# Kernel tuning notes

Measured on AMD Instinct MI355X. Metric: run time of the kernel, lower is better.

## Reference

```python
import jax, jax.numpy as jnp
import numpy as np

DIM = 128
L = 4
EPS = 1e-5


def setup_inputs() -> dict:
    key = jax.random.key(0)
    ks = jax.random.split(key, 16)
    g, n_per = 4096, 32
    n = g * n_per
    e = 4 * n
    s = 0.05
    inp = {
        "x_atoms": jax.random.randint(ks[0], (n, 2), 0, 3),
        "edge_index": jax.random.randint(ks[1], (2, e), 0, n),
        "edge_attr": jax.random.randint(ks[2], (e, 2), 0, 3),
        "batch": jnp.repeat(jnp.arange(g), n_per),
        "num_graphs": g,
        "max_nodes": n_per,
        "task_embs": jax.random.normal(ks[3], (g, DIM), jnp.float32),
        "teb": jax.random.normal(ks[4], (g, DIM), jnp.float32),
        "emb1": jax.random.normal(ks[5], (120, DIM), jnp.float32) * s,
        "emb2": jax.random.normal(ks[6], (3, DIM), jnp.float32) * s,
        "edge_e1": jax.random.normal(ks[7], (L, 6, DIM), jnp.float32) * s,
        "edge_e2": jax.random.normal(ks[8], (L, 3, DIM), jnp.float32) * s,
        "W1": jax.random.normal(ks[9], (L, DIM, 2 * DIM), jnp.float32) * s,
        "b1": jnp.zeros((L, 2 * DIM), jnp.float32),
        "W2": jax.random.normal(ks[10], (L, 2 * DIM, DIM), jnp.float32) * s,
        "b2": jnp.zeros((L, DIM), jnp.float32),
        "bn_w": jnp.ones((L, DIM), jnp.float32),
        "bn_b": jnp.zeros((L, DIM), jnp.float32),
        "film_Wg": jax.random.normal(ks[11], (2, DIM, DIM), jnp.float32) * s,
        "film_bg": jnp.zeros((2, DIM), jnp.float32),
        "film_Wb": jax.random.normal(ks[12], (2, DIM, DIM), jnp.float32) * s,
        "film_bb": jnp.zeros((2, DIM), jnp.float32),
    }
    return inp


def _gin_layer(x, src, dst, eattr, e1, e2, W1, b1, W2, b2):
    # GINConv (pretrain-gnns): scatter-add of (x_j + edge_emb) + self-loop (attr [4,0]), then 2-layer MLP.
    n = x.shape[0]
    emb = e1[eattr[:, 0]] + e2[eattr[:, 1]]                       # [E, D]
    agg = jax.ops.segment_sum(x[src] + emb, dst, num_segments=n)  # [N, D]
    agg = agg + x + (e1[4] + e2[0])                               # self loops
    h = jax.nn.relu(agg @ W1 + b1)
    return h @ W2 + b2


def _batchnorm(x, w, b):
    mu = jnp.mean(x, axis=0)
    var = jnp.var(x, axis=0)
    return (x - mu) * jax.lax.rsqrt(var + EPS) * w + b


def reference(x_atoms, edge_index, edge_attr, batch, num_graphs, max_nodes,
              task_embs, teb, emb1, emb2, edge_e1, edge_e2,
              W1, b1, W2, b2, bn_w, bn_b,
              film_Wg, film_bg, film_Wb, film_bb):
    g = int(num_graphs)
    n = x_atoms.shape[0]
    x = emb1[x_atoms[:, 0]] + emb2[x_atoms[:, 1]]                 # [N, D]
    # --- add virtual nodes (one per graph) and bidirectional virtual edges ---
    x = jnp.concatenate([x, teb], axis=0)                         # [N+g, D]
    dst0 = jnp.arange(n)
    vsrc = n + batch                                              # virtual node index per real node
    src_all = jnp.concatenate([edge_index[0], vsrc, dst0])
    dst_all = jnp.concatenate([edge_index[1], dst0, vsrc])
    v_attr = jnp.tile(jnp.array([[5, 0]], dtype=edge_attr.dtype), (2 * n, 1))
    eattr = jnp.concatenate([edge_attr, v_attr], axis=0)
    # --- positions within graph for to_dense_batch (batch is sorted) ---
    counts = jnp.bincount(batch, length=g)
    offsets = jnp.cumsum(counts) - counts
    pos = dst0 - offsets[batch]
    for layer in range(L):
        x = _gin_layer(x, src_all, dst_all, eattr,
                       edge_e1[layer], edge_e2[layer],
                       W1[layer], b1[layer], W2[layer], b2[layer])
        if layer in (1, 3):
            xv = x[n:]
            dense = jnp.zeros((g, int(max_nodes), DIM), x.dtype).at[batch, pos].set(x[:n])
            fl = layer // 3
            gamma = task_embs @ film_Wg[fl] + film_bg[fl]          # [g, D]
            beta = task_embs @ film_Wb[fl] + film_bb[fl]
            dense = gamma[:, None, :] * dense + beta[:, None, :]
            x = jnp.concatenate([dense[batch, pos], xv], axis=0)   # masked_select inverse
        x = _batchnorm(x, bn_w[layer], bn_b[layer])
        if layer != L - 1:
            x = jax.nn.relu(x)
        # dropout is identity in eval mode
    return x[:n]
```

## Files before the change

kernel.cpp:

```cpp
#include <hip/hip_runtime.h>
#include <hip/hip_bf16.h>

typedef __bf16 bf16_t;
typedef bf16_t bf16x8 __attribute__((ext_vector_type(8)));
typedef float f32x4 __attribute__((ext_vector_type(4)));

#define EPSV 1e-5f

__global__ void k_zerof(float* p, int cnt) {
  int i = blockIdx.x * 256 + threadIdx.x;
  if (i < cnt) p[i] = 0.f;
}
__global__ void k_zeroi(int* p, int cnt) {
  int i = blockIdx.x * 256 + threadIdx.x;
  if (i < cnt) p[i] = 0;
}

__global__ void k_prep_weights(const float* __restrict__ W1, const float* __restrict__ W2,
                               bf16_t* __restrict__ W1T, bf16_t* __restrict__ W2T, int total) {
  int idx = blockIdx.x * 256 + threadIdx.x;
  if (idx >= total) return;
  int l = idx >> 15, r = idx & 32767;
  int k = r >> 8, c = r & 255;
  W1T[(l << 15) + c * 128 + k] = (bf16_t)W1[idx];
  int k2 = r >> 7, c2 = r & 127;
  W2T[(l << 15) + c2 * 256 + k2] = (bf16_t)W2[idx];
}

__global__ void k_prep_film(const float* __restrict__ Wg, const float* __restrict__ Wb,
                            bf16_t* __restrict__ fWT) {
  int idx = blockIdx.x * 256 + threadIdx.x;
  if (idx >= 4 * 16384) return;
  int m = idx >> 14, r = idx & 16383;
  int c = r >> 7, k = r & 127;
  const float* W = ((m & 1) ? Wb : Wg) + (m >> 1) * 16384;
  fWT[idx] = (bf16_t)W[k * 128 + c];
}

__global__ void k_prep_te(const float* __restrict__ te, bf16_t* __restrict__ teb_out, int total) {
  int idx = blockIdx.x * 256 + threadIdx.x;
  if (idx < total) teb_out[idx] = (bf16_t)te[idx];
}

__global__ void k_ecomb(const float* __restrict__ e1, const float* __restrict__ e2,
                        float* __restrict__ ec, int total) {
  int idx = blockIdx.x * 256 + threadIdx.x;
  if (idx >= total) return;
  int ch = idx & 127;
  int t = idx >> 7;
  int comb = t % 18, l = t / 18;
  int i = comb / 3, j = comb % 3;
  ec[idx] = e1[(l * 6 + i) * 128 + ch] + e2[(l * 3 + j) * 128 + ch];
}

__launch_bounds__(256, 2)
__global__ void k_film(const bf16_t* __restrict__ teb, const bf16_t* __restrict__ fWT,
                       const float* __restrict__ bg, const float* __restrict__ bb,
                       float* __restrict__ gbuf, int g) {
  const int mat = blockIdx.x & 3;
  const int r0 = (blockIdx.x >> 2) * 64;
  const int tid = threadIdx.x;
  const int wave = tid >> 6, lane = tid & 63;
  const int lr = lane & 15, lk = lane >> 4;
  const int w32 = wave * 32;
  const bf16_t* W = fWT + mat * 16384;
  const float* B = ((mat & 1) ? bb : bg) + (mat >> 1) * 128;

  bf16x8 bbf[2][4];
  #pragma unroll
  for (int cf = 0; cf < 2; ++cf)
    #pragma unroll
    for (int kk = 0; kk < 4; ++kk)
      bbf[cf][kk] = *(const bf16x8*)(W + ((w32 + cf * 16 + lr) << 7) + kk * 32 + (lk << 3));

  f32x4 acc[4][2];
  f32x4 zero4 = {0.f, 0.f, 0.f, 0.f};
  #pragma unroll
  for (int rf = 0; rf < 4; ++rf)
    #pragma unroll
    for (int cf = 0; cf < 2; ++cf) acc[rf][cf] = zero4;

  #pragma unroll
  for (int kk = 0; kk < 4; ++kk) {
    bf16x8 a[4];
    #pragma unroll
    for (int rf = 0; rf < 4; ++rf)
      a[rf] = *(const bf16x8*)(teb + ((size_t)(r0 + rf * 16 + lr) << 7) + kk * 32 + (lk << 3));
    #pragma unroll
    for (int rf = 0; rf < 4; ++rf)
      #pragma unroll
      for (int cf = 0; cf < 2; ++cf)
        acc[rf][cf] = __builtin_amdgcn_mfma_f32_16x16x32_bf16(a[rf], bbf[cf][kk], acc[rf][cf], 0, 0, 0);
  }

  float* out = gbuf + (size_t)mat * g * 128;
  #pragma unroll
  for (int cf = 0; cf < 2; ++cf) {
    int col = w32 + cf * 16 + lr;
    float bias = B[col];
    #pragma unroll
    for (int rf = 0; rf < 4; ++rf)
      #pragma unroll
      for (int j = 0; j < 4; ++j) {
        int row = r0 + rf * 16 + lk * 4 + j;
        out[(size_t)row * 128 + col] = acc[rf][cf][j] + bias;
      }
  }
}

__global__ void k_init_x(const int* __restrict__ xa, const float* __restrict__ teb,
                         const float* __restrict__ emb1, const float* __restrict__ emb2,
                         bf16_t* __restrict__ x, int n, int N) {
  int idx = blockIdx.x * 256 + threadIdx.x;
  if (idx >= N * 128) return;
  int row = idx >> 7, ch = idx & 127;
  float v;
  if (row < n) v = emb1[xa[row * 2] * 128 + ch] + emb2[xa[row * 2 + 1] * 128 + ch];
  else v = teb[(size_t)(row - n) * 128 + ch];
  x[idx] = (bf16_t)v;
}

__global__ void k_hist(const int* __restrict__ eidx, int* __restrict__ cnt, int E) {
  int i = blockIdx.x * 256 + threadIdx.x;
  if (i < E) atomicAdd(&cnt[eidx[E + i]], 1);
}

__global__ void k_scan1(const int* __restrict__ cnt, int* __restrict__ part,
                        int* __restrict__ bsum, int n) {
  __shared__ int s[256];
  int i = blockIdx.x * 256 + threadIdx.x;
  int v = (i < n) ? cnt[i] : 0;
  s[threadIdx.x] = v;
  for (int off = 1; off < 256; off <<= 1) {
    __syncthreads();
    int t = (threadIdx.x >= off) ? s[threadIdx.x - off] : 0;
    __syncthreads();
    s[threadIdx.x] += t;
  }
  __syncthreads();
  if (i < n) part[i] = s[threadIdx.x] - v;
  if (threadIdx.x == 255) bsum[blockIdx.x] = s[255];
}

__global__ void k_scan2(int* bsum, int nb) {
  __shared__ int s[512];
  int v = ((int)threadIdx.x < nb) ? bsum[threadIdx.x] : 0;
  s[threadIdx.x] = v;
  for (int off = 1; off < 512; off <<= 1) {
    __syncthreads();
    int t = ((int)threadIdx.x >= off) ? s[threadIdx.x - off] : 0;
    __syncthreads();
    s[threadIdx.x] += t;
  }
  __syncthreads();
  if ((int)threadIdx.x < nb) bsum[threadIdx.x] = s[threadIdx.x] - v;
}

__global__ void k_scan3(int* __restrict__ rp, const int* __restrict__ bsum,
                        int* __restrict__ fill, int n, int E) {
  int i = blockIdx.x * 256 + threadIdx.x;
  if (i < n) {
    int v = rp[i] + bsum[i >> 8];
    rp[i] = v;
    fill[i] = v;
  }
  if (i == 0) rp[n] = E;
}

__global__ void k_scatter(const int* __restrict__ eidx, const int* __restrict__ eattr,
                          int* __restrict__ fill, int* __restrict__ pack, int E) {
  int i = blockIdx.x * 256 + threadIdx.x;
  if (i >= E) return;
  int s = eidx[i];
  int d = eidx[E + i];
  int comb = eattr[2 * i] * 3 + eattr[2 * i + 1];
  int p = atomicAdd(&fill[d], 1);
  pack[p] = s | (comb << 20);
}

__global__ void k_normx(const bf16_t* __restrict__ y, const float* __restrict__ scsh,
                        bf16_t* __restrict__ xn, int total8) {
  int i = blockIdx.x * 256 + threadIdx.x;
  if (i >= total8) return;
  int ch8 = i & 15;
  bf16x8 v = ((const bf16x8*)y)[i];
  float4 sc0 = ((const float4*)scsh)[ch8 * 2];
  float4 sc1 = ((const float4*)scsh)[ch8 * 2 + 1];
  float4 sh0 = ((const float4*)(scsh + 128))[ch8 * 2];
  float4 sh1 = ((const float4*)(scsh + 128))[ch8 * 2 + 1];
  float sc[8] = {sc0.x, sc0.y, sc0.z, sc0.w, sc1.x, sc1.y, sc1.z, sc1.w};
  float sh[8] = {sh0.x, sh0.y, sh0.z, sh0.w, sh1.x, sh1.y, sh1.z, sh1.w};
  bf16x8 o;
  #pragma unroll
  for (int j = 0; j < 8; ++j)
    o[j] = (bf16_t)fmaxf(fmaf((float)v[j], sc[j], sh[j]), 0.f);
  ((bf16x8*)xn)[i] = o;
}

__global__ void k_agg(const bf16_t* __restrict__ xn, const int* __restrict__ batch,
                      const int* __restrict__ rp, const int* __restrict__ pack,
                      const float* __restrict__ ec,
                      bf16_t* __restrict__ agg, int n, int N, int npg) {
  int node = blockIdx.x * 16 + (threadIdx.x >> 4);
  if (node >= N) return;
  const int lane = threadIdx.x & 63;
  const int li = lane & 15;
  const int grpl = lane & 48;
  const int ch0 = li * 8;

  float4 s0 = *(const float4*)(ec + 12 * 128 + ch0);
  float4 s1 = *(const float4*)(ec + 12 * 128 + ch0 + 4);
  float4 v0 = *(const float4*)(ec + 15 * 128 + ch0);
  float4 v1 = *(const float4*)(ec + 15 * 128 + ch0 + 4);
  bf16x8 hs = *(const bf16x8*)(xn + ((size_t)node << 7) + ch0);
  float acc[8];

  if (node < n) {
    int b = batch[node];
    bf16x8 hv = *(const bf16x8*)(xn + ((size_t)(n + b) << 7) + ch0);
    acc[0] = (float)hs[0] + (float)hv[0] + s0.x + v0.x;
    acc[1] = (float)hs[1] + (float)hv[1] + s0.y + v0.y;
    acc[2] = (float)hs[2] + (float)hv[2] + s0.z + v0.z;
    acc[3] = (float)hs[3] + (float)hv[3] + s0.w + v0.w;
    acc[4] = (float)hs[4] + (float)hv[4] + s1.x + v1.x;
    acc[5] = (float)hs[5] + (float)hv[5] + s1.y + v1.y;
    acc[6] = (float)hs[6] + (float)hv[6] + s1.z + v1.z;
    acc[7] = (float)hs[7] + (float)hv[7] + s1.w + v1.w;
    int beg = rp[node], end = rp[node + 1];
    for (int base = beg; base < end; base += 16) {
      int cnt = end - base; if (cnt > 16) cnt = 16;
      int pl = pack[base + (li < cnt ? li : cnt - 1)];
      for (int j0 = 0; j0 < cnt; j0 += 4) {
        bf16x8 hx[4]; float4 e0[4], e1[4]; float m[4];
        #pragma unroll
        for (int u = 0; u < 4; ++u) {
          int j = j0 + u;
          int jj = j < cnt ? j : cnt - 1;
          m[u] = (j < cnt) ? 1.f : 0.f;
          int p = __shfl(pl, grpl | jj, 64);
          hx[u] = *(const bf16x8*)(xn + ((size_t)(p & 0xFFFFF) << 7) + ch0);
          const float* er = ec + ((p >> 20) & 31) * 128 + ch0;
          e0[u] = *(const float4*)er;
          e1[u] = *(const float4*)(er + 4);
        }
        #pragma unroll
        for (int u = 0; u < 4; ++u) {
          acc[0] = fmaf(m[u], (float)hx[u][0] + e0[u].x, acc[0]);
          acc[1] = fmaf(m[u], (float)hx[u][1] + e0[u].y, acc[1]);
          acc[2] = fmaf(m[u], (float)hx[u][2] + e0[u].z, acc[2]);
          acc[3] = fmaf(m[u], (float)hx[u][3] + e0[u].w, acc[3]);
          acc[4] = fmaf(m[u], (float)hx[u][4] + e1[u].x, acc[4]);
          acc[5] = fmaf(m[u], (float)hx[u][5] + e1[u].y, acc[5]);
          acc[6] = fmaf(m[u], (float)hx[u][6] + e1[u].z, acc[6]);
          acc[7] = fmaf(m[u], (float)hx[u][7] + e1[u].w, acc[7]);
        }
      }
    }
  } else {
    float fn = (float)npg;
    acc[0] = (float)hs[0] + s0.x + fn * v0.x;
    acc[1] = (float)hs[1] + s0.y + fn * v0.y;
    acc[2] = (float)hs[2] + s0.z + fn * v0.z;
    acc[3] = (float)hs[3] + s0.w + fn * v0.w;
    acc[4] = (float)hs[4] + s1.x + fn * v1.x;
    acc[5] = (float)hs[5] + s1.y + fn * v1.y;
    acc[6] = (float)hs[6] + s1.z + fn * v1.z;
    acc[7] = (float)hs[7] + s1.w + fn * v1.w;
    int base = (node - n) * npg;
    for (int k = 0; k < npg; k += 4) {
      bf16x8 hx[4];
      #pragma unroll
      for (int u = 0; u < 4; ++u)
        hx[u] = *(const bf16x8*)(xn + ((size_t)(base + k + u) << 7) + ch0);
      #pragma unroll
      for (int u = 0; u < 4; ++u)
        #pragma unroll
        for (int j = 0; j < 8; ++j) acc[j] += (float)hx[u][j];
    }
  }

  bf16x8 o;
  #pragma unroll
  for (int j = 0; j < 8; ++j) o[j] = (bf16_t)acc[j];
  *(bf16x8*)(agg + ((size_t)node << 7) + ch0) = o;
}

__launch_bounds__(512, 4)
__global__ void k_mlp(const bf16_t* __restrict__ agg, const bf16_t* __restrict__ W1T,
                      const bf16_t* __restrict__ W2T, const float* __restrict__ b1,
                      const float* __restrict__ b2, const float* __restrict__ gamma,
                      const float* __restrict__ beta, const int* __restrict__ batch,
                      bf16_t* __restrict__ y, float* __restrict__ gstats, int n, int N) {
  __shared__ __align__(16) char As[16384];
  __shared__ __align__(16) char Hs[32768];
  __shared__ float sred[256];
  const int tid = threadIdx.x;
  const int m0 = blockIdx.x * 64;
  const int wave = tid >> 6, lane = tid & 63;
  const int lr = lane & 15, lk = lane >> 4;
  if (tid < 256) sred[tid] = 0.f;

  #pragma unroll
  for (int it = 0; it < 2; ++it) {
    int e = it * 512 + tid;
    int row = e >> 4, c16 = e & 15;
    bf16x8 v = *(const bf16x8*)(agg + ((size_t)(m0 + row) << 7) + c16 * 8);
    int byte = (row << 8) + (c16 << 4);
    byte ^= (row & 7) << 4;
    *(bf16x8*)(As + byte) = v;
  }

  const int c1base = wave * 32;
  bf16x8 bb1[2][4];
  #pragma unroll
  for (int cf = 0; cf < 2; ++cf)
    #pragma unroll
    for (int kk = 0; kk < 4; ++kk)
      bb1[cf][kk] = *(const bf16x8*)(W1T + ((c1base + cf * 16 + lr) << 7) + kk * 32 + (lk << 3));

  __syncthreads();

  f32x4 zero4 = {0.f, 0.f, 0.f, 0.f};
  f32x4 acc1[4][2];
  #pragma unroll
  for (int rf = 0; rf < 4; ++rf)
    #pragma unroll
    for (int cf = 0; cf < 2; ++cf) acc1[rf][cf] = zero4;

  #pragma unroll
  for (int kk = 0; kk < 4; ++kk) {
    bf16x8 a[4];
    #pragma unroll
    for (int rf = 0; rf < 4; ++rf) {
      int arow = rf * 16 + lr;
      int abyte = (arow << 8) + kk * 64 + (lk << 4);
      abyte ^= (arow & 7) << 4;
      a[rf] = *(const bf16x8*)(As + abyte);
    }
    #pragma unroll
    for (int rf = 0; rf < 4; ++rf)
      #pragma unroll
      for (int cf = 0; cf < 2; ++cf)
        acc1[rf][cf] = __builtin_amdgcn_mfma_f32_16x16x32_bf16(a[rf], bb1[cf][kk], acc1[rf][cf], 0, 0, 0);
  }

  #pragma unroll
  for (int cf = 0; cf < 2; ++cf) {
    int col = c1base + cf * 16 + lr;
    float bias = b1[col];
    #pragma unroll
    for (int rf = 0; rf < 4; ++rf)
      #pragma unroll
      for (int j = 0; j < 4; ++j) {
        int r = rf * 16 + lk * 4 + j;
        float h = acc1[rf][cf][j] + bias;
        h = h > 0.f ? h : 0.f;
        int byte = (r << 9) + col * 2;
        byte ^= (r & 15) << 4;
        *(bf16_t*)(Hs + byte) = (bf16_t)h;
      }
  }

  const int c2base = wave * 16;
  bf16x8 bb2[8];
  #pragma unroll
  for (int kk = 0; kk < 8; ++kk)
    bb2[kk] = *(const bf16x8*)(W2T + ((c2base + lr) << 8) + kk * 32 + (lk << 3));

  __syncthreads();

  f32x4 acc2[4];
  #pragma unroll
  for (int rf = 0; rf < 4; ++rf) acc2[rf] = zero4;

  #pragma unroll
  for (int kk = 0; kk < 8; ++kk) {
    bf16x8 a2[4];
    #pragma unroll
    for (int rf = 0; rf < 4; ++rf) {
      int row = rf * 16 + lr;
      int byte = (row << 9) + kk * 64 + (lk << 4);
      byte ^= (row & 15) << 4;
      a2[rf] = *(const bf16x8*)(Hs + byte);
    }
    #pragma unroll
    for (int rf = 0; rf < 4; ++rf)
      acc2[rf] = __builtin_amdgcn_mfma_f32_16x16x32_bf16(a2[rf], bb2[kk], acc2[rf], 0, 0, 0);
  }

  int gb[4][4];
  #pragma unroll
  for (int rf = 0; rf < 4; ++rf)
    #pragma unroll
    for (int j = 0; j < 4; ++j) {
      int row = m0 + rf * 16 + lk * 4 + j;
      gb[rf][j] = (gamma != nullptr && row < n) ? batch[row] : -1;
    }

  {
    int col = c2base + lr;
    float bias = b2[col];
    float s = 0.f, q = 0.f;
    #pragma unroll
    for (int rf = 0; rf < 4; ++rf)
      #pragma unroll
      for (int j = 0; j < 4; ++j) {
        int row = m0 + rf * 16 + lk * 4 + j;
        float v = acc2[rf][j] + bias;
        if (gb[rf][j] >= 0)
          v = gamma[(size_t)gb[rf][j] * 128 + col] * v + beta[(size_t)gb[rf][j] * 128 + col];
        y[(size_t)row * 128 + col] = (bf16_t)v;
        s += v; q += v * v;
      }
    s += __shfl_xor(s, 16, 64); s += __shfl_xor(s, 32, 64);
    q += __shfl_xor(q, 16, 64); q += __shfl_xor(q, 32, 64);
    if (lane < 16) { sred[col] = s; sred[128 + col] = q; }
  }
  __syncthreads();
  if (tid < 256) atomicAdd(&gstats[((blockIdx.x & 15) << 8) + tid], sred[tid]);
}

__global__ void k_finalize(float* st, const float* __restrict__ bnw,
                           const float* __restrict__ bnb, float invN) {
  int ch = threadIdx.x;
  float s = 0.f, q = 0.f;
  #pragma unroll
  for (int c = 0; c < 16; ++c) { s += st[c * 256 + ch]; q += st[c * 256 + 128 + ch]; }
  __syncthreads();
  #pragma unroll
  for (int z = 0; z < 32; ++z) st[ch * 32 + z] = 0.f;
  float mean = s * invN;
  float var = fmaxf(q * invN - mean * mean, 0.f);
  float inv = rsqrtf(var + EPSV);
  float sc = inv * bnw[ch];
  st[4096 + ch] = sc;
  st[4224 + ch] = bnb[ch] - mean * sc;
}

__global__ void k_norm(const bf16_t* __restrict__ yin, const float* __restrict__ scsh,
                       float* __restrict__ out, int total8) {
  int i = blockIdx.x * 256 + threadIdx.x;
  if (i >= total8) return;
  int ch8 = i & 15;
  bf16x8 v = ((const bf16x8*)yin)[i];
  float4 sc0 = ((const float4*)scsh)[ch8 * 2];
  float4 sc1 = ((const float4*)scsh)[ch8 * 2 + 1];
  float4 sh0 = ((const float4*)(scsh + 128))[ch8 * 2];
  float4 sh1 = ((const float4*)(scsh + 128))[ch8 * 2 + 1];
  float4 r0, r1;
  r0.x = (float)v[0] * sc0.x + sh0.x;
  r0.y = (float)v[1] * sc0.y + sh0.y;
  r0.z = (float)v[2] * sc0.z + sh0.z;
  r0.w = (float)v[3] * sc0.w + sh0.w;
  r1.x = (float)v[4] * sc1.x + sh1.x;
  r1.y = (float)v[5] * sc1.y + sh1.y;
  r1.z = (float)v[6] * sc1.z + sh1.z;
  r1.w = (float)v[7] * sc1.w + sh1.w;
  ((float4*)out)[i * 2] = r0;
  ((float4*)out)[i * 2 + 1] = r1;
}

extern "C" void kernel_launch(void* const* d_in, const int* in_sizes, int n_in,
                              void* d_out, int out_size, void* d_ws, size_t ws_size,
                              hipStream_t stream) {
  const int*   x_atoms    = (const int*)d_in[0];
  const int*   edge_index = (const int*)d_in[1];
  const int*   edge_attr  = (const int*)d_in[2];
  const int*   batch      = (const int*)d_in[3];
  const float* task_embs  = (const float*)d_in[6];
  const float* teb        = (const float*)d_in[7];
  const float* emb1       = (const float*)d_in[8];
  const float* emb2       = (const float*)d_in[9];
  const float* edge_e1    = (const float*)d_in[10];
  const float* edge_e2    = (const float*)d_in[11];
  const float* W1         = (const float*)d_in[12];
  const float* b1         = (const float*)d_in[13];
  const float* W2         = (const float*)d_in[14];
  const float* b2         = (const float*)d_in[15];
  const float* bnw        = (const float*)d_in[16];
  const float* bnb        = (const float*)d_in[17];
  const float* fWg        = (const float*)d_in[18];
  const float* fbg        = (const float*)d_in[19];
  const float* fWb        = (const float*)d_in[20];
  const float* fbb        = (const float*)d_in[21];

  const int n   = in_sizes[0] / 2;
  const int E   = in_sizes[1] / 2;
  const int g   = in_sizes[6] / 128;
  const int N   = n + g;
  const int npg = n / g;
  const int L   = in_sizes[12] / 32768;

  char* ws = (char*)d_ws;
  size_t off = 0;
  auto alloc = [&](size_t bytes) { size_t o = off; off += (bytes + 255) & ~(size_t)255; return o; };
  bf16_t* xbuf   = (bf16_t*)(ws + alloc((size_t)N * 128 * 2));
  bf16_t* xn     = (bf16_t*)(ws + alloc((size_t)N * 128 * 2));
  bf16_t* aggb   = (bf16_t*)(ws + alloc((size_t)N * 128 * 2));
  float*  gbuf   = (float*)(ws + alloc((size_t)4 * g * 128 * 4));
  bf16_t* W1Tb   = (bf16_t*)(ws + alloc((size_t)L * 32768 * 2));
  bf16_t* W2Tb   = (bf16_t*)(ws + alloc((size_t)L * 32768 * 2));
  bf16_t* fWTb   = (bf16_t*)(ws + alloc((size_t)4 * 16384 * 2));
  bf16_t* tebuf  = (bf16_t*)(ws + alloc((size_t)g * 128 * 2));
  float*  ecomb  = (float*)(ws + alloc((size_t)L * 18 * 128 * 4));
  float*  gstats = (float*)(ws + alloc((size_t)(4096 + 256) * 4));
  int*    row_ptr= (int*)(ws + alloc((size_t)(n + 1) * 4));
  int*    fill   = (int*)(ws + alloc((size_t)n * 4));
  int*    epack  = (int*)(ws + alloc((size_t)E * 4));
  int*    bsum   = (int*)(ws + alloc(512 * 4));
  (void)ws_size; (void)n_in; (void)out_size;

  k_prep_weights<<<(L * 32768 + 255) / 256, 256, 0, stream>>>(W1, W2, W1Tb, W2Tb, L * 32768);
  k_prep_film<<<(4 * 16384 + 255) / 256, 256, 0, stream>>>(fWg, fWb, fWTb);
  k_prep_te<<<(g * 128 + 255) / 256, 256, 0, stream>>>(task_embs, tebuf, g * 128);
  k_init_x<<<(N * 128 + 255) / 256, 256, 0, stream>>>(x_atoms, teb, emb1, emb2, xn, n, N);
  k_ecomb<<<(L * 18 * 128 + 255) / 256, 256, 0, stream>>>(edge_e1, edge_e2, ecomb, L * 18 * 128);
  k_film<<<(g / 64) * 4, 256, 0, stream>>>(tebuf, fWTb, fbg, fbb, gbuf, g);

  const int nb = (n + 255) / 256;
  k_zeroi<<<nb, 256, 0, stream>>>(fill, n);
  k_hist<<<(E + 255) / 256, 256, 0, stream>>>(edge_index, fill, E);
  k_scan1<<<nb, 256, 0, stream>>>(fill, row_ptr, bsum, n);
  k_scan2<<<1, 512, 0, stream>>>(bsum, nb);
  k_scan3<<<nb, 256, 0, stream>>>(row_ptr, bsum, fill, n, E);
  k_scatter<<<(E + 255) / 256, 256, 0, stream>>>(edge_index, edge_attr, fill, epack, E);

  k_zerof<<<16, 256, 0, stream>>>(gstats, 4096);
  for (int l = 0; l < 4; ++l) {
    if (l > 0)
      k_normx<<<(N * 16 + 255) / 256, 256, 0, stream>>>(xbuf, gstats + 4096, xn, N * 16);
    k_agg<<<(N + 15) / 16, 256, 0, stream>>>(xn, batch, row_ptr, epack,
        ecomb + (size_t)l * 18 * 128, aggb, n, N, npg);
    const float* gm = nullptr; const float* bt = nullptr;
    if (l == 1) { gm = gbuf;                       bt = gbuf + (size_t)g * 128; }
    if (l == 3) { gm = gbuf + (size_t)2 * g * 128; bt = gbuf + (size_t)3 * g * 128; }
    k_mlp<<<(N + 63) / 64, 512, 0, stream>>>(aggb, W1Tb + (size_t)l * 32768,
        W2Tb + (size_t)l * 32768, b1 + l * 256, b2 + l * 128, gm, bt, batch,
        xbuf, gstats, n, N);
    k_finalize<<<1, 128, 0, stream>>>(gstats, bnw + l * 128, bnb + l * 128, 1.0f / (float)N);
  }
  k_norm<<<(n * 16 + 255) / 256, 256, 0, stream>>>(xbuf, gstats + 4096, (float*)d_out, n * 16);
}
```

Before: 531.8 us.

## Make MLP kernel persistent with double-buffered prefetch of next input tile

Turns the fused two-layer MLP kernel into a grid-stride persistent kernel capped at 512 blocks. W1 fragments are loaded once per block, and the next 64-row tile of aggregated features is prefetched into registers and written to a second shared-memory buffer while the current tile's epilogue runs. The aim is to amortise weight loads and hide global-load latency behind MFMA work. In exchange it doubles the input-tile shared memory, which may reduce occupancy, and adds row bounds checks.

```diff
diff --git a/kernel.cpp b/kernel.cpp
--- a/kernel.cpp
+++ b/kernel.cpp
@@ -290,25 +290,16 @@
                       const bf16_t* __restrict__ W2T, const float* __restrict__ b1,
                       const float* __restrict__ b2, const float* __restrict__ gamma,
                       const float* __restrict__ beta, const int* __restrict__ batch,
-                      bf16_t* __restrict__ y, float* __restrict__ gstats, int n, int N) {
-  __shared__ __align__(16) char As[16384];
+                      bf16_t* __restrict__ y, float* __restrict__ gstats,
+                      int n, int N, int ntiles) {
+  __shared__ __align__(16) char As[2][16384];
   __shared__ __align__(16) char Hs[32768];
   __shared__ float sred[256];
   const int tid = threadIdx.x;
-  const int m0 = blockIdx.x * 64;
   const int wave = tid >> 6, lane = tid & 63;
   const int lr = lane & 15, lk = lane >> 4;
-  if (tid < 256) sred[tid] = 0.f;
-
-  #pragma unroll
-  for (int it = 0; it < 2; ++it) {
-    int e = it * 512 + tid;
-    int row = e >> 4, c16 = e & 15;
-    bf16x8 v = *(const bf16x8*)(agg + ((size_t)(m0 + row) << 7) + c16 * 8);
-    int byte = (row << 8) + (c16 << 4);
-    byte ^= (row & 7) << 4;
-    *(bf16x8*)(As + byte) = v;
-  }
+  const int srow = tid >> 4;
+  const int sc16 = tid & 15;
 
   const int c1base = wave * 32;
   bf16x8 bb1[2][4];
@@ -317,107 +308,148 @@
     #pragma unroll
     for (int kk = 0; kk < 4; ++kk)
       bb1[cf][kk] = *(const bf16x8*)(W1T + ((c1base + cf * 16 + lr) << 7) + kk * 32 + (lk << 3));
-
+  const int c2base = wave * 16;
+
+  int t = blockIdx.x;
+  {
+    int m0 = t * 64;
+    #pragma unroll
+    for (int it = 0; it < 2; ++it) {
+      int row = it * 32 + srow;
+      int r = m0 + row; r = r < N ? r : N - 1;
+      bf16x8 v = *(const bf16x8*)(agg + ((size_t)r << 7) + sc16 * 8);
+      int byte = (row << 8) + (sc16 << 4);
+      byte ^= (row & 7) << 4;
+      *(bf16x8*)(As[0] + byte) = v;
+    }
+  }
   __syncthreads();
 
   f32x4 zero4 = {0.f, 0.f, 0.f, 0.f};
-  f32x4 acc1[4][2];
-  #pragma unroll
-  for (int rf = 0; rf < 4; ++rf)
-    #pragma unroll
-    for (int cf = 0; cf < 2; ++cf) acc1[rf][cf] = zero4;
-
-  #pragma unroll
-  for (int kk = 0; kk < 4; ++kk) {
-    bf16x8 a[4];
-    #pragma unroll
-    for (int rf = 0; rf < 4; ++rf) {
-      int arow = rf * 16 + lr;
-      int abyte = (arow << 8) + kk * 64 + (lk << 4);
-      abyte ^= (arow & 7) << 4;
-      a[rf] = *(const bf16x8*)(As + abyte);
-    }
+  int cur = 0;
+  for (; t < ntiles; t += gridDim.x) {
+    const int m0 = t * 64;
+
+    f32x4 acc1[4][2];
     #pragma unroll
     for (int rf = 0; rf < 4; ++rf)
       #pragma unroll
-      for (int cf = 0; cf < 2; ++cf)
-        acc1[rf][cf] = __builtin_amdgcn_mfma_f32_16x16x32_bf16(a[rf], bb1[cf][kk], acc1[rf][cf], 0, 0, 0);
-  }
-
-  #pragma unroll
-  for (int cf = 0; cf < 2; ++cf) {
-    int col = c1base + cf * 16 + lr;
-    float bias = b1[col];
-    #pragma unroll
-    for (int rf = 0; rf < 4; ++rf)
-      #pragma unroll
-      for (int j = 0; j < 4; ++j) {
-        int r = rf * 16 + lk * 4 + j;
-        float h = acc1[rf][cf][j] + bias;
-        h = h > 0.f ? h : 0.f;
-        int byte = (r << 9) + col * 2;
-        byte ^= (r & 15) << 4;
-        *(bf16_t*)(Hs + byte) = (bf16_t)h;
-      }
-  }
-
-  const int c2base = wave * 16;
-  bf16x8 bb2[8];
-  #pragma unroll
-  for (int kk = 0; kk < 8; ++kk)
-    bb2[kk] = *(const bf16x8*)(W2T + ((c2base + lr) << 8) + kk * 32 + (lk << 3));
-
-  __syncthreads();
-
-  f32x4 acc2[4];
-  #pragma unroll
-  for (int rf = 0; rf < 4; ++rf) acc2[rf] = zero4;
-
-  #pragma unroll
-  for (int kk = 0; kk < 8; ++kk) {
-    bf16x8 a2[4];
-    #pragma unroll
-    for (int rf = 0; rf < 4; ++rf) {
-      int row = rf * 16 + lr;
-      int byte = (row << 9) + kk * 64 + (lk << 4);
-      byte ^= (row & 15) << 4;
-      a2[rf] = *(const bf16x8*)(Hs + byte);
-    }
-    #pragma unroll
-    for (int rf = 0; rf < 4; ++rf)
-      acc2[rf] = __builtin_amdgcn_mfma_f32_16x16x32_bf16(a2[rf], bb2[kk], acc2[rf], 0, 0, 0);
-  }
-
-  int gb[4][4];
-  #pragma unroll
-  for (int rf = 0; rf < 4; ++rf)
-    #pragma unroll
-    for (int j = 0; j < 4; ++j) {
-      int row = m0 + rf * 16 + lk * 4 + j;
-      gb[rf][j] = (gamma != nullptr && row < n) ? batch[row] : -1;
-    }
-
-  {
-    int col = c2base + lr;
-    float bias = b2[col];
-    float s = 0.f, q = 0.f;
+      for (int cf = 0; cf < 2; ++cf) acc1[rf][cf] = zero4;
+    #pragma unroll
+    for (int kk = 0; kk < 4; ++kk) {
+      bf16x8 a[4];
+      #pragma unroll
+      for (int rf = 0; rf < 4; ++rf) {
+        int arow = rf * 16 + lr;
+        int abyte = (arow << 8) + kk * 64 + (lk << 4);
+        abyte ^= (arow & 7) << 4;
+        a[rf] = *(const bf16x8*)(As[cur] + abyte);
+      }
+      #pragma unroll
+      for (int rf = 0; rf < 4; ++rf)
+        #pragma unroll
+        for (int cf = 0; cf < 2; ++cf)
+          acc1[rf][cf] = __builtin_amdgcn_mfma_f32_16x16x32_bf16(a[rf], bb1[cf][kk], acc1[rf][cf], 0, 0, 0);
+    }
+
+    #pragma unroll
+    for (int cf = 0; cf < 2; ++cf) {
+      int col = c1base + cf * 16 + lr;
+      float bias = b1[col];
+      #pragma unroll
+      for (int rf = 0; rf < 4; ++rf)
+        #pragma unroll
+        for (int j = 0; j < 4; ++j) {
+          int r = rf * 16 + lk * 4 + j;
+          float h = acc1[rf][cf][j] + bias;
+          h = h > 0.f ? h : 0.f;
+          int byte = (r << 9) + col * 2;
+          byte ^= (r & 15) << 4;
+          *(bf16_t*)(Hs + byte) = (bf16_t)h;
+        }
+    }
+
+    bf16x8 bb2[8];
+    #pragma unroll
+    for (int kk = 0; kk < 8; ++kk)
+      bb2[kk] = *(const bf16x8*)(W2T + ((c2base + lr) << 8) + kk * 32 + (lk << 3));
+
+    __syncthreads();
+
+    f32x4 acc2[4];
+    #pragma unroll
+    for (int rf = 0; rf < 4; ++rf) acc2[rf] = zero4;
+    #pragma unroll
+    for (int kk = 0; kk < 8; ++kk) {
+      bf16x8 a2[4];
+      #pragma unroll
+      for (int rf = 0; rf < 4; ++rf) {
+        int row = rf * 16 + lr;
+        int byte = (row << 9) + kk * 64 + (lk << 4);
+        byte ^= (row & 15) << 4;
+        a2[rf] = *(const bf16x8*)(Hs + byte);
+      }
+      #pragma unroll
+      for (int rf = 0; rf < 4; ++rf)
+        acc2[rf] = __builtin_amdgcn_mfma_f32_16x16x32_bf16(a2[rf], bb2[kk], acc2[rf], 0, 0, 0);
+    }
+
+    int tn = t + gridDim.x;
+    bf16x8 st[2];
+    if (tn < ntiles) {
+      int m0n = tn * 64;
+      #pragma unroll
+      for (int it = 0; it < 2; ++it) {
+        int row = it * 32 + srow;
+        int r = m0n + row; r = r < N ? r : N - 1;
+        st[it] = *(const bf16x8*)(agg + ((size_t)r << 7) + sc16 * 8);
+      }
+    }
+
+    int gb[4][4];
     #pragma unroll
     for (int rf = 0; rf < 4; ++rf)
       #pragma unroll
       for (int j = 0; j < 4; ++j) {
         int row = m0 + rf * 16 + lk * 4 + j;
-        float v = acc2[rf][j] + bias;
-        if (gb[rf][j] >= 0)
-          v = gamma[(size_t)gb[rf][j] * 128 + col] * v + beta[(size_t)gb[rf][j] * 128 + col];
-        y[(size_t)row * 128 + col] = (bf16_t)v;
-        s += v; q += v * v;
-      }
-    s += __shfl_xor(s, 16, 64); s += __shfl_xor(s, 32, 64);
-    q += __shfl_xor(q, 16, 64); q += __shfl_xor(q, 32, 64);
-    if (lane < 16) { sred[col] = s; sred[128 + col] = q; }
-  }
-  __syncthreads();
-  if (tid < 256) atomicAdd(&gstats[((blockIdx.x & 15) << 8) + tid], sred[tid]);
+        gb[rf][j] = (gamma != nullptr && row < n) ? batch[row] : -1;
+      }
+    {
+      int col = c2base + lr;
+      float bias = b2[col];
+      float s = 0.f, q = 0.f;
+      #pragma unroll
+      for (int rf = 0; rf < 4; ++rf)
+        #pragma unroll
+        for (int j = 0; j < 4; ++j) {
+          int row = m0 + rf * 16 + lk * 4 + j;
+          if (row < N) {
+            float v = acc2[rf][j] + bias;
+            if (gb[rf][j] >= 0)
+              v = gamma[(size_t)gb[rf][j] * 128 + col] * v + beta[(size_t)gb[rf][j] * 128 + col];
+            y[(size_t)row * 128 + col] = (bf16_t)v;
+            s += v; q += v * v;
+          }
+        }
+      s += __shfl_xor(s, 16, 64); s += __shfl_xor(s, 32, 64);
+      q += __shfl_xor(q, 16, 64); q += __shfl_xor(q, 32, 64);
+      if (lane < 16) { sred[col] = s; sred[128 + col] = q; }
+    }
+
+    if (tn < ntiles) {
+      #pragma unroll
+      for (int it = 0; it < 2; ++it) {
+        int row = it * 32 + srow;
+        int byte = (row << 8) + (sc16 << 4);
+        byte ^= (row & 7) << 4;
+        *(bf16x8*)(As[cur ^ 1] + byte) = st[it];
+      }
+    }
+    __syncthreads();
+
+    if (tid < 256) atomicAdd(&gstats[((t & 15) << 8) + tid], sred[tid]);
+    cur ^= 1;
+  }
 }
 
 __global__ void k_finalize(float* st, const float* __restrict__ bnw,
@@ -490,13 +522,14 @@
   const int N   = n + g;
   const int npg = n / g;
   const int L   = in_sizes[12] / 32768;
+  const int ntiles = (N + 63) / 64;
 
   char* ws = (char*)d_ws;
   size_t off = 0;
   auto alloc = [&](size_t bytes) { size_t o = off; off += (bytes + 255) & ~(size_t)255; return o; };
   bf16_t* xbuf   = (bf16_t*)(ws + alloc((size_t)N * 128 * 2));
   bf16_t* xn     = (bf16_t*)(ws + alloc((size_t)N * 128 * 2));
-  bf16_t* aggb   = (bf16_t*)(ws + alloc((size_t)N * 128 * 2));
+  bf16_t* aggb   = (bf16_t*)(ws + alloc((size_t)(ntiles * 64) * 128 * 2));
   float*  gbuf   = (float*)(ws + alloc((size_t)4 * g * 128 * 4));
   bf16_t* W1Tb   = (bf16_t*)(ws + alloc((size_t)L * 32768 * 2));
   bf16_t* W2Tb   = (bf16_t*)(ws + alloc((size_t)L * 32768 * 2));
@@ -526,6 +559,7 @@
   k_scatter<<<(E + 255) / 256, 256, 0, stream>>>(edge_index, edge_attr, fill, epack, E);
 
   k_zerof<<<16, 256, 0, stream>>>(gstats, 4096);
+  const int mlp_grid = (ntiles < 512) ? ntiles : 512;
   for (int l = 0; l < 4; ++l) {
     if (l > 0)
       k_normx<<<(N * 16 + 255) / 256, 256, 0, stream>>>(xbuf, gstats + 4096, xn, N * 16);
@@ -534,9 +568,9 @@
     const float* gm = nullptr; const float* bt = nullptr;
     if (l == 1) { gm = gbuf;                       bt = gbuf + (size_t)g * 128; }
     if (l == 3) { gm = gbuf + (size_t)2 * g * 128; bt = gbuf + (size_t)3 * g * 128; }
-    k_mlp<<<(N + 63) / 64, 512, 0, stream>>>(aggb, W1Tb + (size_t)l * 32768,
+    k_mlp<<<mlp_grid, 512, 0, stream>>>(aggb, W1Tb + (size_t)l * 32768,
         W2Tb + (size_t)l * 32768, b1 + l * 256, b2 + l * 128, gm, bt, batch,
-        xbuf, gstats, n, N);
+        xbuf, gstats, n, N, ntiles);
     k_finalize<<<1, 128, 0, stream>>>(gstats, bnw + l * 128, bnb + l * 128, 1.0f / (float)N);
   }
   k_norm<<<(n * 16 + 255) / 256, 256, 0, stream>>>(xbuf, gstats + 4096, (float*)d_out, n * 16);
```

After: 1.082 ms. +103.4%, slower.

## Fuse batchnorm+ReLU into aggregation gather and merge prep kernels

Applied to the files above, without the earlier changes.

Removes the separate normalize-and-ReLU pass that wrote a normalized copy of x each layer, and instead applies the batchnorm scale/shift and ReLU on the fly inside the aggregation kernel on every gathered neighbor row. This saves one full read and write of the N×128 activation per layer and three kernel launches per forward. The cost is extra FMAs per gathered edge, since each node is normalized about five times instead of once. It also merges the four small weight and embedding prep kernels into a single launch.

```diff
diff --git a/kernel.cpp b/kernel.cpp
--- a/kernel.cpp
+++ b/kernel.cpp
@@ -16,41 +16,41 @@
   if (i < cnt) p[i] = 0;
 }
 
-__global__ void k_prep_weights(const float* __restrict__ W1, const float* __restrict__ W2,
-                               bf16_t* __restrict__ W1T, bf16_t* __restrict__ W2T, int total) {
+__global__ void k_prep_all(const float* __restrict__ W1, const float* __restrict__ W2,
+                           bf16_t* __restrict__ W1T, bf16_t* __restrict__ W2T,
+                           const float* __restrict__ Wg, const float* __restrict__ Wb,
+                           bf16_t* __restrict__ fWT,
+                           const float* __restrict__ te, bf16_t* __restrict__ teb,
+                           const float* __restrict__ e1, const float* __restrict__ e2,
+                           float* __restrict__ ec, int L, int g) {
   int idx = blockIdx.x * 256 + threadIdx.x;
-  if (idx >= total) return;
-  int l = idx >> 15, r = idx & 32767;
-  int k = r >> 8, c = r & 255;
-  W1T[(l << 15) + c * 128 + k] = (bf16_t)W1[idx];
-  int k2 = r >> 7, c2 = r & 127;
-  W2T[(l << 15) + c2 * 256 + k2] = (bf16_t)W2[idx];
-}
-
-__global__ void k_prep_film(const float* __restrict__ Wg, const float* __restrict__ Wb,
-                            bf16_t* __restrict__ fWT) {
-  int idx = blockIdx.x * 256 + threadIdx.x;
-  if (idx >= 4 * 16384) return;
-  int m = idx >> 14, r = idx & 16383;
-  int c = r >> 7, k = r & 127;
-  const float* W = ((m & 1) ? Wb : Wg) + (m >> 1) * 16384;
-  fWT[idx] = (bf16_t)W[k * 128 + c];
-}
-
-__global__ void k_prep_te(const float* __restrict__ te, bf16_t* __restrict__ teb_out, int total) {
-  int idx = blockIdx.x * 256 + threadIdx.x;
-  if (idx < total) teb_out[idx] = (bf16_t)te[idx];
-}
-
-__global__ void k_ecomb(const float* __restrict__ e1, const float* __restrict__ e2,
-                        float* __restrict__ ec, int total) {
-  int idx = blockIdx.x * 256 + threadIdx.x;
-  if (idx >= total) return;
-  int ch = idx & 127;
-  int t = idx >> 7;
-  int comb = t % 18, l = t / 18;
-  int i = comb / 3, j = comb % 3;
-  ec[idx] = e1[(l * 6 + i) * 128 + ch] + e2[(l * 3 + j) * 128 + ch];
+  int base0 = L * 32768;
+  int base1 = base0 + 4 * 16384;
+  int base2 = base1 + g * 128;
+  int base3 = base2 + L * 18 * 128;
+  if (idx < base0) {
+    int l = idx >> 15, r = idx & 32767;
+    int k = r >> 8, c = r & 255;
+    W1T[(l << 15) + c * 128 + k] = (bf16_t)W1[idx];
+    int k2 = r >> 7, c2 = r & 127;
+    W2T[(l << 15) + c2 * 256 + k2] = (bf16_t)W2[idx];
+  } else if (idx < base1) {
+    int i2 = idx - base0;
+    int m = i2 >> 14, r = i2 & 16383;
+    int c = r >> 7, k = r & 127;
+    const float* W = ((m & 1) ? Wb : Wg) + (m >> 1) * 16384;
+    fWT[i2] = (bf16_t)W[k * 128 + c];
+  } else if (idx < base2) {
+    int i2 = idx - base1;
+    teb[i2] = (bf16_t)te[i2];
+  } else if (idx < base3) {
+    int i2 = idx - base2;
+    int ch = i2 & 127;
+    int t = i2 >> 7;
+    int comb = t % 18, l = t / 18;
+    int i = comb / 3, j = comb % 3;
+    ec[i2] = e1[(l * 6 + i) * 128 + ch] + e2[(l * 3 + j) * 128 + ch];
+  }
 }
 
 __launch_bounds__(256, 2)
@@ -178,28 +178,10 @@
   pack[p] = s | (comb << 20);
 }
 
-__global__ void k_normx(const bf16_t* __restrict__ y, const float* __restrict__ scsh,
-                        bf16_t* __restrict__ xn, int total8) {
-  int i = blockIdx.x * 256 + threadIdx.x;
-  if (i >= total8) return;
-  int ch8 = i & 15;
-  bf16x8 v = ((const bf16x8*)y)[i];
-  float4 sc0 = ((const float4*)scsh)[ch8 * 2];
-  float4 sc1 = ((const float4*)scsh)[ch8 * 2 + 1];
-  float4 sh0 = ((const float4*)(scsh + 128))[ch8 * 2];
-  float4 sh1 = ((const float4*)(scsh + 128))[ch8 * 2 + 1];
-  float sc[8] = {sc0.x, sc0.y, sc0.z, sc0.w, sc1.x, sc1.y, sc1.z, sc1.w};
-  float sh[8] = {sh0.x, sh0.y, sh0.z, sh0.w, sh1.x, sh1.y, sh1.z, sh1.w};
-  bf16x8 o;
-  #pragma unroll
-  for (int j = 0; j < 8; ++j)
-    o[j] = (bf16_t)fmaxf(fmaf((float)v[j], sc[j], sh[j]), 0.f);
-  ((bf16x8*)xn)[i] = o;
-}
-
-__global__ void k_agg(const bf16_t* __restrict__ xn, const int* __restrict__ batch,
+template <bool NM>
+__global__ void k_agg(const bf16_t* __restrict__ x, const int* __restrict__ batch,
                       const int* __restrict__ rp, const int* __restrict__ pack,
-                      const float* __restrict__ ec,
+                      const float* __restrict__ ec, const float* __restrict__ scsh,
                       bf16_t* __restrict__ agg, int n, int N, int npg) {
   int node = blockIdx.x * 16 + (threadIdx.x >> 4);
   if (node >= N) return;
@@ -208,24 +190,34 @@
   const int grpl = lane & 48;
   const int ch0 = li * 8;
 
+  float sc[8], sh[8];
+  if (NM) {
+    float4 a0 = *(const float4*)(scsh + ch0);
+    float4 a1 = *(const float4*)(scsh + ch0 + 4);
+    float4 b0 = *(const float4*)(scsh + 128 + ch0);
+    float4 b1 = *(const float4*)(scsh + 128 + ch0 + 4);
+    sc[0]=a0.x; sc[1]=a0.y; sc[2]=a0.z; sc[3]=a0.w;
+    sc[4]=a1.x; sc[5]=a1.y; sc[6]=a1.z; sc[7]=a1.w;
+    sh[0]=b0.x; sh[1]=b0.y; sh[2]=b0.z; sh[3]=b0.w;
+    sh[4]=b1.x; sh[5]=b1.y; sh[6]=b1.z; sh[7]=b1.w;
+  }
+  #define NRM(v, j) (NM ? fmaxf(fmaf((v), sc[j], sh[j]), 0.f) : (v))
+
   float4 s0 = *(const float4*)(ec + 12 * 128 + ch0);
   float4 s1 = *(const float4*)(ec + 12 * 128 + ch0 + 4);
   float4 v0 = *(const float4*)(ec + 15 * 128 + ch0);
   float4 v1 = *(const float4*)(ec + 15 * 128 + ch0 + 4);
-  bf16x8 hs = *(const bf16x8*)(xn + ((size_t)node << 7) + ch0);
+  float se[8] = {s0.x, s0.y, s0.z, s0.w, s1.x, s1.y, s1.z, s1.w};
+  float ve[8] = {v0.x, v0.y, v0.z, v0.w, v1.x, v1.y, v1.z, v1.w};
+  bf16x8 hs = *(const bf16x8*)(x + ((size_t)node << 7) + ch0);
   float acc[8];
 
   if (node < n) {
     int b = batch[node];
-    bf16x8 hv = *(const bf16x8*)(xn + ((size_t)(n + b) << 7) + ch0);
-    acc[0] = (float)hs[0] + (float)hv[0] + s0.x + v0.x;
-    acc[1] = (float)hs[1] + (float)hv[1] + s0.y + v0.y;
-    acc[2] = (float)hs[2] + (float)hv[2] + s0.z + v0.z;
-    acc[3] = (float)hs[3] + (float)hv[3] + s0.w + v0.w;
-    acc[4] = (float)hs[4] + (float)hv[4] + s1.x + v1.x;
-    acc[5] = (float)hs[5] + (float)hv[5] + s1.y + v1.y;
-    acc[6] = (float)hs[6] + (float)hv[6] + s1.z + v1.z;
-    acc[7] = (float)hs[7] + (float)hv[7] + s1.w + v1.w;
+    bf16x8 hv = *(const bf16x8*)(x + ((size_t)(n + b) << 7) + ch0);
+    #pragma unroll
+    for (int j = 0; j < 8; ++j)
+      acc[j] = NRM((float)hs[j], j) + NRM((float)hv[j], j) + se[j] + ve[j];
     int beg = rp[node], end = rp[node + 1];
     for (int base = beg; base < end; base += 16) {
       int cnt = end - base; if (cnt > 16) cnt = 16;
@@ -238,46 +230,39 @@
           int jj = j < cnt ? j : cnt - 1;
           m[u] = (j < cnt) ? 1.f : 0.f;
           int p = __shfl(pl, grpl | jj, 64);
-          hx[u] = *(const bf16x8*)(xn + ((size_t)(p & 0xFFFFF) << 7) + ch0);
+          hx[u] = *(const bf16x8*)(x + ((size_t)(p & 0xFFFFF) << 7) + ch0);
           const float* er = ec + ((p >> 20) & 31) * 128 + ch0;
           e0[u] = *(const float4*)er;
           e1[u] = *(const float4*)(er + 4);
         }
         #pragma unroll
         for (int u = 0; u < 4; ++u) {
-          acc[0] = fmaf(m[u], (float)hx[u][0] + e0[u].x, acc[0]);
-          acc[1] = fmaf(m[u], (float)hx[u][1] + e0[u].y, acc[1]);
-          acc[2] = fmaf(m[u], (float)hx[u][2] + e0[u].z, acc[2]);
-          acc[3] = fmaf(m[u], (float)hx[u][3] + e0[u].w, acc[3]);
-          acc[4] = fmaf(m[u], (float)hx[u][4] + e1[u].x, acc[4]);
-          acc[5] = fmaf(m[u], (float)hx[u][5] + e1[u].y, acc[5]);
-          acc[6] = fmaf(m[u], (float)hx[u][6] + e1[u].z, acc[6]);
-          acc[7] = fmaf(m[u], (float)hx[u][7] + e1[u].w, acc[7]);
+          float ee[8] = {e0[u].x, e0[u].y, e0[u].z, e0[u].w,
+                         e1[u].x, e1[u].y, e1[u].z, e1[u].w};
+          #pragma unroll
+          for (int j = 0; j < 8; ++j)
+            acc[j] = fmaf(m[u], NRM((float)hx[u][j], j) + ee[j], acc[j]);
         }
       }
     }
   } else {
     float fn = (float)npg;
-    acc[0] = (float)hs[0] + s0.x + fn * v0.x;
-    acc[1] = (float)hs[1] + s0.y + fn * v0.y;
-    acc[2] = (float)hs[2] + s0.z + fn * v0.z;
-    acc[3] = (float)hs[3] + s0.w + fn * v0.w;
-    acc[4] = (float)hs[4] + s1.x + fn * v1.x;
-    acc[5] = (float)hs[5] + s1.y + fn * v1.y;
-    acc[6] = (float)hs[6] + s1.z + fn * v1.z;
-    acc[7] = (float)hs[7] + s1.w + fn * v1.w;
+    #pragma unroll
+    for (int j = 0; j < 8; ++j)
+      acc[j] = NRM((float)hs[j], j) + se[j] + fn * ve[j];
     int base = (node - n) * npg;
     for (int k = 0; k < npg; k += 4) {
       bf16x8 hx[4];
       #pragma unroll
       for (int u = 0; u < 4; ++u)
-        hx[u] = *(const bf16x8*)(xn + ((size_t)(base + k + u) << 7) + ch0);
+        hx[u] = *(const bf16x8*)(x + ((size_t)(base + k + u) << 7) + ch0);
       #pragma unroll
       for (int u = 0; u < 4; ++u)
         #pragma unroll
-        for (int j = 0; j < 8; ++j) acc[j] += (float)hx[u][j];
+        for (int j = 0; j < 8; ++j) acc[j] += NRM((float)hx[u][j], j);
     }
   }
+  #undef NRM
 
   bf16x8 o;
   #pragma unroll
@@ -495,7 +480,6 @@
   size_t off = 0;
   auto alloc = [&](size_t bytes) { size_t o = off; off += (bytes + 255) & ~(size_t)255; return o; };
   bf16_t* xbuf   = (bf16_t*)(ws + alloc((size_t)N * 128 * 2));
-  bf16_t* xn     = (bf16_t*)(ws + alloc((size_t)N * 128 * 2));
   bf16_t* aggb   = (bf16_t*)(ws + alloc((size_t)N * 128 * 2));
   float*  gbuf   = (float*)(ws + alloc((size_t)4 * g * 128 * 4));
   bf16_t* W1Tb   = (bf16_t*)(ws + alloc((size_t)L * 32768 * 2));
@@ -510,11 +494,10 @@
   int*    bsum   = (int*)(ws + alloc(512 * 4));
   (void)ws_size; (void)n_in; (void)out_size;
 
-  k_prep_weights<<<(L * 32768 + 255) / 256, 256, 0, stream>>>(W1, W2, W1Tb, W2Tb, L * 32768);
-  k_prep_film<<<(4 * 16384 + 255) / 256, 256, 0, stream>>>(fWg, fWb, fWTb);
-  k_prep_te<<<(g * 128 + 255) / 256, 256, 0, stream>>>(task_embs, tebuf, g * 128);
-  k_init_x<<<(N * 128 + 255) / 256, 256, 0, stream>>>(x_atoms, teb, emb1, emb2, xn, n, N);
-  k_ecomb<<<(L * 18 * 128 + 255) / 256, 256, 0, stream>>>(edge_e1, edge_e2, ecomb, L * 18 * 128);
+  const int prep_total = L * 32768 + 4 * 16384 + g * 128 + L * 18 * 128;
+  k_prep_all<<<(prep_total + 255) / 256, 256, 0, stream>>>(W1, W2, W1Tb, W2Tb,
+      fWg, fWb, fWTb, task_embs, tebuf, edge_e1, edge_e2, ecomb, L, g);
+  k_init_x<<<(N * 128 + 255) / 256, 256, 0, stream>>>(x_atoms, teb, emb1, emb2, xbuf, n, N);
   k_film<<<(g / 64) * 4, 256, 0, stream>>>(tebuf, fWTb, fbg, fbb, gbuf, g);
 
   const int nb = (n + 255) / 256;
@@ -527,10 +510,13 @@
 
   k_zerof<<<16, 256, 0, stream>>>(gstats, 4096);
   for (int l = 0; l < 4; ++l) {
-    if (l > 0)
-      k_normx<<<(N * 16 + 255) / 256, 256, 0, stream>>>(xbuf, gstats + 4096, xn, N * 16);
-    k_agg<<<(N + 15) / 16, 256, 0, stream>>>(xn, batch, row_ptr, epack,
-        ecomb + (size_t)l * 18 * 128, aggb, n, N, npg);
+    const float* scsh = gstats + 4096;
+    if (l == 0)
+      k_agg<false><<<(N + 15) / 16, 256, 0, stream>>>(xbuf, batch, row_ptr, epack,
+          ecomb + (size_t)l * 18 * 128, nullptr, aggb, n, N, npg);
+    else
+      k_agg<true><<<(N + 15) / 16, 256, 0, stream>>>(xbuf, batch, row_ptr, epack,
+          ecomb + (size_t)l * 18 * 128, scsh, aggb, n, N, npg);
     const float* gm = nullptr; const float* bt = nullptr;
     if (l == 1) { gm = gbuf;                       bt = gbuf + (size_t)g * 128; }
     if (l == 3) { gm = gbuf + (size_t)2 * g * 128; bt = gbuf + (size_t)3 * g * 128; }
```

New measurement: 541.4 us. Within noise of the previous version (+1.8%).
